# Kernel tuning notes

Hardware: AMD Instinct MI355X
Metric: run time of the kernel (lower is better)

## Reference

```python
import jax, jax.numpy as jnp
import numpy as np

IN_FEATURES = 4096
PADDED = 4096               # padded_dim == in_features -> no crop
K_HALF = PADDED // 2 + 1    # 2049
K = 1024                    # truncation: only first K half-spectrum coeffs active
BATCH = 8192


def setup_inputs() -> dict:
    key = jax.random.key(0)
    k1, k2, k3, k4 = jax.random.split(key, 4)
    x = jax.random.normal(k1, (BATCH, IN_FEATURES), dtype=jnp.float32)
    w_real = jax.random.normal(k2, (K_HALF,), dtype=jnp.float32) * 0.1
    w_imag = jax.random.normal(k3, (K_HALF,), dtype=jnp.float32) * 0.1
    # DC and Nyquist bins must be real (Hermitian spectrum of a real filter)
    w_imag = w_imag.at[0].set(0.0).at[-1].set(0.0)
    bias = jax.random.normal(k4, (), dtype=jnp.float32) * 0.1
    return {"x": x, "w_real": w_real, "w_imag": w_imag, "bias": bias}


def _fft_full(w_real, w_imag):
    # K-truncated half spectrum -> full Hermitian-symmetric spectrum (PADDED even)
    mask = (jnp.arange(K_HALF) < K).astype(w_real.dtype)
    half = w_real * mask + 1j * (w_imag * mask)            # (K_HALF,) complex
    nyq = half[-1].real[None].astype(half.dtype)           # real Nyquist bin
    full = jnp.concatenate([half[:-1], nyq, jnp.conj(half[1:-1])[::-1]])
    return full                                            # (PADDED,) complex


def reference(x, w_real, w_imag, bias):
    # in_features == padded_dim: no padding, no crop
    fft_full = _fft_full(w_real, w_imag)
    Xf = jnp.fft.fft(x, axis=-1, norm="ortho")             # (B, PADDED) complex
    y = jnp.fft.ifft(Xf * fft_full, axis=-1, norm="ortho").real
    return y + bias                                        # scalar bias (vector_bias=False)
```

## Files before the change

kernel.cpp:

```cpp
#include <hip/hip_runtime.h>

#define NT 256

__device__ __forceinline__ int PH(int l) { return l + 2 * (l >> 4); }

template<bool INV>
__device__ __forceinline__ void dft16(float* vr, float* vi) {
    constexpr float C1 = 0.9238795325112867f;
    constexpr float S1 = 0.3826834323650898f;
    constexpr float HF = 0.7071067811865476f;
    const float WR[10] = {1.f,  C1,  HF,  S1, 0.f, 0.f, -HF, 0.f, 0.f, -C1};
    const float WI[10] = {0.f, -S1, -HF, -C1, -1.f, 0.f, -HF, 0.f, 0.f,  S1};

    float ar[16], ai[16];
    #pragma unroll
    for (int jl = 0; jl < 4; ++jl) {
        float x0r = vr[jl],      x0i = vi[jl];
        float x1r = vr[jl + 4],  x1i = vi[jl + 4];
        float x2r = vr[jl + 8],  x2i = vi[jl + 8];
        float x3r = vr[jl + 12], x3i = vi[jl + 12];
        float t0r = x0r + x2r, t0i = x0i + x2i;
        float t1r = x0r - x2r, t1i = x0i - x2i;
        float t2r = x1r + x3r, t2i = x1i + x3i;
        float t3r = x1r - x3r, t3i = x1i - x3i;
        ar[jl]     = t0r + t2r;  ai[jl]     = t0i + t2i;
        ar[jl + 8] = t0r - t2r;  ai[jl + 8] = t0i - t2i;
        if (!INV) {
            ar[jl + 4]  = t1r + t3i;  ai[jl + 4]  = t1i - t3r;
            ar[jl + 12] = t1r - t3i;  ai[jl + 12] = t1i + t3r;
        } else {
            ar[jl + 4]  = t1r - t3i;  ai[jl + 4]  = t1i + t3r;
            ar[jl + 12] = t1r + t3i;  ai[jl + 12] = t1i - t3r;
        }
    }
    #pragma unroll
    for (int k4 = 1; k4 < 4; ++k4) {
        #pragma unroll
        for (int jl = 1; jl < 4; ++jl) {
            const int e = jl * k4;
            float wr = WR[e];
            float wi = INV ? -WI[e] : WI[e];
            const int id = jl + 4 * k4;
            float xr = ar[id], xi = ai[id];
            ar[id] = xr * wr - xi * wi;
            ai[id] = xr * wi + xi * wr;
        }
    }
    #pragma unroll
    for (int k4 = 0; k4 < 4; ++k4) {
        float x0r = ar[4*k4 + 0], x0i = ai[4*k4 + 0];
        float x1r = ar[4*k4 + 1], x1i = ai[4*k4 + 1];
        float x2r = ar[4*k4 + 2], x2i = ai[4*k4 + 2];
        float x3r = ar[4*k4 + 3], x3i = ai[4*k4 + 3];
        float t0r = x0r + x2r, t0i = x0i + x2i;
        float t1r = x0r - x2r, t1i = x0i - x2i;
        float t2r = x1r + x3r, t2i = x1i + x3i;
        float t3r = x1r - x3r, t3i = x1i - x3i;
        vr[k4]     = t0r + t2r;  vi[k4]     = t0i + t2i;
        vr[k4 + 8] = t0r - t2r;  vi[k4 + 8] = t0i - t2i;
        if (!INV) {
            vr[k4 + 4]  = t1r + t3i;  vi[k4 + 4]  = t1i - t3r;
            vr[k4 + 12] = t1r - t3i;  vi[k4 + 12] = t1i + t3r;
        } else {
            vr[k4 + 4]  = t1r - t3i;  vi[k4 + 4]  = t1i + t3r;
            vr[k4 + 12] = t1r + t3i;  vi[k4 + 12] = t1i - t3r;
        }
    }
}

__device__ __forceinline__ void apply_tw_powers(float* vr, float* vi, float wr, float wi) {
    const float w2r = wr * wr - wi * wi;
    const float w2i = 2.0f * wr * wi;
    float aor = wr,  aoi = wi;
    float aer = w2r, aei = w2i;
    #pragma unroll
    for (int e = 1; e < 16; e += 2) {
        { float xr = vr[e], xi = vi[e];
          vr[e] = xr * aor - xi * aoi;
          vi[e] = xr * aoi + xi * aor; }
        if (e + 1 < 16) {
            float xr = vr[e + 1], xi = vi[e + 1];
            vr[e + 1] = xr * aer - xi * aei;
            vi[e + 1] = xr * aei + xi * aer;
        }
        if (e + 2 < 16) {
            float nr = aor * w2r - aoi * w2i, ni = aor * w2i + aoi * w2r;
            aor = nr; aoi = ni;
            nr = aer * w2r - aei * w2i; ni = aer * w2i + aei * w2r;
            aer = nr; aei = ni;
        }
    }
}

__global__ __launch_bounds__(NT, 4) void spectral_circulant_r16v3(
    const float* __restrict__ x,
    const float* __restrict__ w_real,
    const float* __restrict__ w_imag,
    const float* __restrict__ bias_p,
    float* __restrict__ out)
{
    __shared__ __align__(16) float2 lds[4606];

    const int t   = threadIdx.x;
    const int blk = blockIdx.x;

    float vr[16], vi[16];

    const float* __restrict__ xa = x + (size_t)(2 * blk) * 4096;
    const float* __restrict__ xb = xa + 4096;
    #pragma unroll
    for (int j = 0; j < 16; ++j) {
        vr[j] = xa[(j << 8) + t];
        vi[j] = xb[(j << 8) + t];
    }

    dft16<false>(vr, vi);
    float sA, cA;
    __sincosf((float)t * -1.5339807878856412e-3f, &sA, &cA);
    apply_tw_powers(vr, vi, cA, sA);

    {
        const int tp = t + 2 * (t >> 4);
        #pragma unroll
        for (int a = 0; a < 16; ++a)
            lds[288 * a + tp] = make_float2(vr[a], vi[a]);
    }
    __syncthreads();

    const int ax = t >> 4;
    const int m2 = t & 15;
    const int base = 288 * ax + m2;

    #pragma unroll
    for (int q = 0; q < 16; ++q) {
        float2 v = lds[base + 18 * q];
        vr[q] = v.x; vi[q] = v.y;
    }

    dft16<false>(vr, vi);
    float sB, cB;
    __sincosf((float)m2 * -2.454369260617026e-2f, &sB, &cB);
    apply_tw_powers(vr, vi, cB, sB);

    #pragma unroll
    for (int b = 0; b < 16; ++b)
        lds[base + 18 * b] = make_float2(vr[b], vi[b]);
    __builtin_amdgcn_wave_barrier();

    const float4* __restrict__ pfr = (const float4*)&lds[288 * ax + 18 * m2];
    #pragma unroll
    for (int m = 0; m < 16; m += 2) {
        float4 v = pfr[m >> 1];
        vr[m] = v.x;     vi[m] = v.y;
        vr[m + 1] = v.z; vi[m + 1] = v.w;
    }

    dft16<false>(vr, vi);

    {
        const int c = (m2 << 4) | ax;
        const float sc = 1.0f / 4096.0f;
        #pragma unroll
        for (int r3 = 0; r3 < 4; ++r3) {
            const int k = (r3 << 8) + c;
            float hr = w_real[k] * sc;
            float hi = w_imag[k] * sc;
            float xr = vr[r3], xi = vi[r3];
            vr[r3] = xr * hr - xi * hi;
            vi[r3] = xr * hi + xi * hr;
        }
        #pragma unroll
        for (int r3 = 4; r3 < 12; ++r3) {
            vr[r3] = 0.0f; vi[r3] = 0.0f;
        }
        {
            const int idx = 1024 - c;
            const float m = (c > 0) ? sc : 0.0f;
            float hr = w_real[idx] * m;
            float hi = -w_imag[idx] * m;
            float xr = vr[12], xi = vi[12];
            vr[12] = xr * hr - xi * hi;
            vi[12] = xr * hi + xi * hr;
        }
        #pragma unroll
        for (int r3 = 13; r3 < 16; ++r3) {
            const int idx = ((16 - r3) << 8) - c;
            float hr = w_real[idx] * sc;
            float hi = -w_imag[idx] * sc;
            float xr = vr[r3], xi = vi[r3];
            vr[r3] = xr * hr - xi * hi;
            vi[r3] = xr * hi + xi * hr;
        }
    }


    dft16<true>(vr, vi);

    {
        float4* __restrict__ pfw = (float4*)&lds[288 * ax + 18 * m2];
        #pragma unroll
        for (int m = 0; m < 16; m += 2)
            pfw[m >> 1] = make_float4(vr[m], vi[m], vr[m + 1], vi[m + 1]);
    }
    __builtin_amdgcn_wave_barrier();

    #pragma unroll
    for (int b = 0; b < 16; ++b) {
        float2 v = lds[base + 18 * b];
        vr[b] = v.x; vi[b] = v.y;
    }

    apply_tw_powers(vr, vi, cB, -sB);
    dft16<true>(vr, vi);

    #pragma unroll
    for (int q = 0; q < 16; ++q)
        lds[base + 18 * q] = make_float2(vr[q], vi[q]);
    __syncthreads();

    {
        const int tp = t + 2 * (t >> 4);
        #pragma unroll
        for (int a = 0; a < 16; ++a) {
            float2 v = lds[288 * a + tp];
            vr[a] = v.x; vi[a] = v.y;
        }
    }

    apply_tw_powers(vr, vi, cA, -sA);
    dft16<true>(vr, vi);

    const float bv = bias_p[0];
    float* __restrict__ oa = out + (size_t)(2 * blk) * 4096;
    float* __restrict__ ob = oa + 4096;
    #pragma unroll
    for (int j = 0; j < 16; ++j) {
        __builtin_nontemporal_store(vr[j] + bv, &oa[(j << 8) + t]);
        __builtin_nontemporal_store(vi[j] + bv, &ob[(j << 8) + t]);
    }
}

extern "C" void kernel_launch(void* const* d_in, const int* in_sizes, int n_in,
                              void* d_out, int out_size, void* d_ws, size_t ws_size,
                              hipStream_t stream) {
    (void)in_sizes; (void)n_in; (void)d_ws; (void)ws_size; (void)out_size;
    const float* x      = (const float*)d_in[0];
    const float* w_real = (const float*)d_in[1];
    const float* w_imag = (const float*)d_in[2];
    const float* bias   = (const float*)d_in[3];
    float* out = (float*)d_out;

    spectral_circulant_r16v3<<<8192 / 2, NT, 0, stream>>>(x, w_real, w_imag, bias, out);
}
```

Measured before the change: 240.4 us.

## Process two complex FFT pairs per block with XOR-swizzled shared memory

Each block now handles four rows (two packed complex signals) instead of two, running every FFT stage twice per thread so twiddle computation, weight loads and barriers are shared across both. The padded shared-memory layout is replaced by an XOR swizzle so the buffer holds two signals without padding. The change aims to raise instruction-level parallelism and amortise per-block overhead. In exchange it doubles register pressure (launch bounds lowered to 2 blocks per SIMD), doubles LDS per block and halves the grid size, which may reduce occupancy.

New measurement: 248.5 us. 3.4% more time.

```diff
diff --git a/kernel.cpp b/kernel.cpp
--- a/kernel.cpp
+++ b/kernel.cpp
@@ -2,7 +2,6 @@
 
 #define NT 256
 
-__device__ __forceinline__ int PH(int l) { return l + 2 * (l >> 4); }
 
 template<bool INV>
 __device__ __forceinline__ void dft16(float* vr, float* vi) {
@@ -68,20 +67,26 @@
     }
 }
 
-__device__ __forceinline__ void apply_tw_powers(float* vr, float* vi, float wr, float wi) {
+__device__ __forceinline__ void cmul_ip(float& xr, float& xi, float wr, float wi) {
+    float r = xr * wr - xi * wi;
+    float i = xr * wi + xi * wr;
+    xr = r; xi = i;
+}
+
+__device__ __forceinline__ void apply_tw_dual(float* vr1, float* vi1,
+                                              float* vr2, float* vi2,
+                                              float wr, float wi) {
     const float w2r = wr * wr - wi * wi;
     const float w2i = 2.0f * wr * wi;
     float aor = wr,  aoi = wi;
     float aer = w2r, aei = w2i;
     #pragma unroll
     for (int e = 1; e < 16; e += 2) {
-        { float xr = vr[e], xi = vi[e];
-          vr[e] = xr * aor - xi * aoi;
-          vi[e] = xr * aoi + xi * aor; }
+        cmul_ip(vr1[e], vi1[e], aor, aoi);
+        cmul_ip(vr2[e], vi2[e], aor, aoi);
         if (e + 1 < 16) {
-            float xr = vr[e + 1], xi = vi[e + 1];
-            vr[e + 1] = xr * aer - xi * aei;
-            vi[e + 1] = xr * aei + xi * aer;
+            cmul_ip(vr1[e + 1], vi1[e + 1], aer, aei);
+            cmul_ip(vr2[e + 1], vi2[e + 1], aer, aei);
         }
         if (e + 2 < 16) {
             float nr = aor * w2r - aoi * w2i, ni = aor * w2i + aoi * w2r;
@@ -92,70 +97,86 @@
     }
 }
 
-__global__ __launch_bounds__(NT, 4) void spectral_circulant_r16v3(
+__global__ __launch_bounds__(NT, 2) void spectral_circulant_r16x2(
     const float* __restrict__ x,
     const float* __restrict__ w_real,
     const float* __restrict__ w_imag,
     const float* __restrict__ bias_p,
     float* __restrict__ out)
 {
-    __shared__ __align__(16) float2 lds[4606];
+    __shared__ __align__(16) float4 lds4[4096];
+    float2* const p2 = (float2*)lds4;
 
     const int t   = threadIdx.x;
     const int blk = blockIdx.x;
 
-    float vr[16], vi[16];
-
-    const float* __restrict__ xa = x + (size_t)(2 * blk) * 4096;
-    const float* __restrict__ xb = xa + 4096;
+    float vr1[16], vi1[16], vr2[16], vi2[16];
+
+    const float* __restrict__ xa = x + (size_t)(4 * blk) * 4096;
     #pragma unroll
     for (int j = 0; j < 16; ++j) {
-        vr[j] = xa[(j << 8) + t];
-        vi[j] = xb[(j << 8) + t];
-    }
-
-    dft16<false>(vr, vi);
+        vr1[j] = xa[(j << 8) + t];
+        vi1[j] = xa[4096 + (j << 8) + t];
+    }
+    #pragma unroll
+    for (int j = 0; j < 16; ++j) {
+        vr2[j] = xa[8192 + (j << 8) + t];
+        vi2[j] = xa[12288 + (j << 8) + t];
+    }
+
+    dft16<false>(vr1, vi1);
+    dft16<false>(vr2, vi2);
     float sA, cA;
     __sincosf((float)t * -1.5339807878856412e-3f, &sA, &cA);
-    apply_tw_powers(vr, vi, cA, sA);
-
-    {
-        const int tp = t + 2 * (t >> 4);
-        #pragma unroll
-        for (int a = 0; a < 16; ++a)
-            lds[288 * a + tp] = make_float2(vr[a], vi[a]);
+    apply_tw_dual(vr1, vi1, vr2, vi2, cA, sA);
+
+    const int e1w = 2 * (((t >> 1) ^ ((t >> 4) & 7))) + (t & 1);
+    #pragma unroll
+    for (int a = 0; a < 16; ++a) {
+        p2[256 * a + e1w]        = make_float2(vr1[a], vi1[a]);
+        p2[4096 + 256 * a + e1w] = make_float2(vr2[a], vi2[a]);
     }
     __syncthreads();
 
     const int ax = t >> 4;
     const int m2 = t & 15;
-    const int base = 288 * ax + m2;
+    const int mh = m2 >> 1, ml = m2 & 1;
+    const int bx = 256 * ax + ml;
 
     #pragma unroll
     for (int q = 0; q < 16; ++q) {
-        float2 v = lds[base + 18 * q];
-        vr[q] = v.x; vi[q] = v.y;
-    }
-
-    dft16<false>(vr, vi);
+        const int ad = bx + 16 * q + 2 * (mh ^ (q & 7));
+        float2 v1 = p2[ad];        vr1[q] = v1.x; vi1[q] = v1.y;
+        float2 v2 = p2[4096 + ad]; vr2[q] = v2.x; vi2[q] = v2.y;
+    }
+
+    dft16<false>(vr1, vi1);
+    dft16<false>(vr2, vi2);
     float sB, cB;
     __sincosf((float)m2 * -2.454369260617026e-2f, &sB, &cB);
-    apply_tw_powers(vr, vi, cB, sB);
-
-    #pragma unroll
-    for (int b = 0; b < 16; ++b)
-        lds[base + 18 * b] = make_float2(vr[b], vi[b]);
+    apply_tw_dual(vr1, vi1, vr2, vi2, cB, sB);
+
+    #pragma unroll
+    for (int b = 0; b < 16; ++b) {
+        const int ad = bx + 16 * b + 2 * (mh ^ (b & 7));
+        p2[ad]        = make_float2(vr1[b], vi1[b]);
+        p2[4096 + ad] = make_float2(vr2[b], vi2[b]);
+    }
     __builtin_amdgcn_wave_barrier();
 
-    const float4* __restrict__ pfr = (const float4*)&lds[288 * ax + 18 * m2];
-    #pragma unroll
-    for (int m = 0; m < 16; m += 2) {
-        float4 v = pfr[m >> 1];
-        vr[m] = v.x;     vi[m] = v.y;
-        vr[m + 1] = v.z; vi[m + 1] = v.w;
-    }
-
-    dft16<false>(vr, vi);
+    const int base4 = 128 * ax + 8 * m2;
+    const int h3 = m2 & 7;
+    #pragma unroll
+    for (int u = 0; u < 8; ++u) {
+        const int F = base4 + (u ^ h3);
+        float4 v1 = lds4[F];
+        vr1[2*u] = v1.x; vi1[2*u] = v1.y; vr1[2*u+1] = v1.z; vi1[2*u+1] = v1.w;
+        float4 v2 = lds4[2048 + F];
+        vr2[2*u] = v2.x; vi2[2*u] = v2.y; vr2[2*u+1] = v2.z; vi2[2*u+1] = v2.w;
+    }
+
+    dft16<false>(vr1, vi1);
+    dft16<false>(vr2, vi2);
 
     {
         const int c = (m2 << 4) | ax;
@@ -163,80 +184,80 @@
         #pragma unroll
         for (int r3 = 0; r3 < 4; ++r3) {
             const int k = (r3 << 8) + c;
-            float hr = w_real[k] * sc;
-            float hi = w_imag[k] * sc;
-            float xr = vr[r3], xi = vi[r3];
-            vr[r3] = xr * hr - xi * hi;
-            vi[r3] = xr * hi + xi * hr;
+            const float hr = w_real[k] * sc, hi = w_imag[k] * sc;
+            cmul_ip(vr1[r3], vi1[r3], hr, hi);
+            cmul_ip(vr2[r3], vi2[r3], hr, hi);
         }
         #pragma unroll
         for (int r3 = 4; r3 < 12; ++r3) {
-            vr[r3] = 0.0f; vi[r3] = 0.0f;
+            vr1[r3] = 0.0f; vi1[r3] = 0.0f;
+            vr2[r3] = 0.0f; vi2[r3] = 0.0f;
         }
         {
             const int idx = 1024 - c;
             const float m = (c > 0) ? sc : 0.0f;
-            float hr = w_real[idx] * m;
-            float hi = -w_imag[idx] * m;
-            float xr = vr[12], xi = vi[12];
-            vr[12] = xr * hr - xi * hi;
-            vi[12] = xr * hi + xi * hr;
+            const float hr = w_real[idx] * m, hi = -w_imag[idx] * m;
+            cmul_ip(vr1[12], vi1[12], hr, hi);
+            cmul_ip(vr2[12], vi2[12], hr, hi);
         }
         #pragma unroll
         for (int r3 = 13; r3 < 16; ++r3) {
             const int idx = ((16 - r3) << 8) - c;
-            float hr = w_real[idx] * sc;
-            float hi = -w_imag[idx] * sc;
-            float xr = vr[r3], xi = vi[r3];
-            vr[r3] = xr * hr - xi * hi;
-            vi[r3] = xr * hi + xi * hr;
-        }
-    }
-
-
-    dft16<true>(vr, vi);
-
-    {
-        float4* __restrict__ pfw = (float4*)&lds[288 * ax + 18 * m2];
-        #pragma unroll
-        for (int m = 0; m < 16; m += 2)
-            pfw[m >> 1] = make_float4(vr[m], vi[m], vr[m + 1], vi[m + 1]);
+            const float hr = w_real[idx] * sc, hi = -w_imag[idx] * sc;
+            cmul_ip(vr1[r3], vi1[r3], hr, hi);
+            cmul_ip(vr2[r3], vi2[r3], hr, hi);
+        }
+    }
+
+
+    dft16<true>(vr1, vi1);
+    dft16<true>(vr2, vi2);
+
+    #pragma unroll
+    for (int u = 0; u < 8; ++u) {
+        const int F = base4 + (u ^ h3);
+        lds4[F]        = make_float4(vr1[2*u], vi1[2*u], vr1[2*u+1], vi1[2*u+1]);
+        lds4[2048 + F] = make_float4(vr2[2*u], vi2[2*u], vr2[2*u+1], vi2[2*u+1]);
     }
     __builtin_amdgcn_wave_barrier();
 
     #pragma unroll
     for (int b = 0; b < 16; ++b) {
-        float2 v = lds[base + 18 * b];
-        vr[b] = v.x; vi[b] = v.y;
-    }
-
-    apply_tw_powers(vr, vi, cB, -sB);
-    dft16<true>(vr, vi);
-
-    #pragma unroll
-    for (int q = 0; q < 16; ++q)
-        lds[base + 18 * q] = make_float2(vr[q], vi[q]);
+        const int ad = bx + 16 * b + 2 * (mh ^ (b & 7));
+        float2 v1 = p2[ad];        vr1[b] = v1.x; vi1[b] = v1.y;
+        float2 v2 = p2[4096 + ad]; vr2[b] = v2.x; vi2[b] = v2.y;
+    }
+
+    apply_tw_dual(vr1, vi1, vr2, vi2, cB, -sB);
+    dft16<true>(vr1, vi1);
+    dft16<true>(vr2, vi2);
+
+    #pragma unroll
+    for (int q = 0; q < 16; ++q) {
+        const int ad = bx + 16 * q + 2 * (mh ^ (q & 7));
+        p2[ad]        = make_float2(vr1[q], vi1[q]);
+        p2[4096 + ad] = make_float2(vr2[q], vi2[q]);
+    }
     __syncthreads();
 
-    {
-        const int tp = t + 2 * (t >> 4);
-        #pragma unroll
-        for (int a = 0; a < 16; ++a) {
-            float2 v = lds[288 * a + tp];
-            vr[a] = v.x; vi[a] = v.y;
-        }
-    }
-
-    apply_tw_powers(vr, vi, cA, -sA);
-    dft16<true>(vr, vi);
+    #pragma unroll
+    for (int a = 0; a < 16; ++a) {
+        float2 v1 = p2[256 * a + e1w];        vr1[a] = v1.x; vi1[a] = v1.y;
+        float2 v2 = p2[4096 + 256 * a + e1w]; vr2[a] = v2.x; vi2[a] = v2.y;
+    }
+
+    apply_tw_dual(vr1, vi1, vr2, vi2, cA, -sA);
+    dft16<true>(vr1, vi1);
+    dft16<true>(vr2, vi2);
 
     const float bv = bias_p[0];
-    float* __restrict__ oa = out + (size_t)(2 * blk) * 4096;
-    float* __restrict__ ob = oa + 4096;
+    float* __restrict__ oa = out + (size_t)(4 * blk) * 4096;
     #pragma unroll
     for (int j = 0; j < 16; ++j) {
-        __builtin_nontemporal_store(vr[j] + bv, &oa[(j << 8) + t]);
-        __builtin_nontemporal_store(vi[j] + bv, &ob[(j << 8) + t]);
+        __builtin_nontemporal_store(vr1[j] + bv, &oa[(j << 8) + t]);
+        __builtin_nontemporal_store(vi1[j] + bv, &oa[4096 + (j << 8) + t]);
+        __builtin_nontemporal_store(vr2[j] + bv, &oa[8192 + (j << 8) + t]);
+        __builtin_nontemporal_store(vi2[j] + bv, &oa[12288 + (j << 8) + t]);
     }
 }
 
@@ -250,5 +271,5 @@
     const float* bias   = (const float*)d_in[3];
     float* out = (float*)d_out;
 
-    spectral_circulant_r16v3<<<8192 / 2, NT, 0, stream>>>(x, w_real, w_imag, bias, out);
-}
+    spectral_circulant_r16x2<<<8192 / 4, NT, 0, stream>>>(x, w_real, w_imag, bias, out);
+}
```
